# Performance work log

Measured on AMD Instinct MI355X. Metric: run time of the kernel, lower is better.

The kernel has to match this reference:

```python
import jax, jax.numpy as jnp
import numpy as np

DIM = 128      # d_msa
HEADS = 8
DH = 64        # dim_head
INNER = HEADS * DH  # 512
R = 64         # tie_attn_dim (MSA rows)
N = 512        # residues
DPAIR = 128
LN_EPS = 1e-5


def _layernorm(x, g, b):
    mu = jnp.mean(x, axis=-1, keepdims=True)
    var = jnp.mean((x - mu) ** 2, axis=-1, keepdims=True)
    return (x - mu) * jax.lax.rsqrt(var + LN_EPS) * g + b


def setup_inputs() -> dict:
    key = jax.random.key(0)
    ks = jax.random.split(key, 12)
    s = 0.02
    return {
        "x": jax.random.normal(ks[0], (R, N, DIM), jnp.float32),
        "pair_bias": jax.random.normal(ks[1], (1, N, N, DPAIR), jnp.float32),
        "Wq": jax.random.normal(ks[2], (DIM, INNER), jnp.float32) * s,
        "Wkv": jax.random.normal(ks[3], (DIM, 2 * INNER), jnp.float32) * s,
        "Wo": jax.random.normal(ks[4], (INNER, DIM), jnp.float32) * s,
        "bo": jnp.zeros((DIM,), jnp.float32),
        "ln_g": jnp.ones((DPAIR,), jnp.float32),
        "ln_b": jnp.zeros((DPAIR,), jnp.float32),
        "Wpair": jax.random.normal(ks[5], (DPAIR, HEADS), jnp.float32) * s,
        "Wsq": jax.random.normal(ks[6], (DIM, DIM), jnp.float32) * s,
        "bsq": jnp.zeros((DIM,), jnp.float32),
        "Wsk": jax.random.normal(ks[7], (DIM, DIM), jnp.float32) * s,
        "bsk": jnp.zeros((DIM,), jnp.float32),
        "tie_attn_dim": R,
    }


def reference(x, pair_bias, Wq, Wkv, Wo, bo, ln_g, ln_b, Wpair, Wsq, bsq, Wsk, bsk, tie_attn_dim):
    r = tie_attn_dim
    br, n, dim = x.shape
    b = br // r
    h, dh = HEADS, DH
    dsw = dim // h  # per-head dim inside PositionalWiseWeight

    # projections: (b*r, n, inner) -> (b, r, h, n, dh)
    q = (x @ Wq).reshape(b, r, n, h, dh).transpose(0, 1, 3, 2, 4)
    kv = x @ Wkv
    k, v = jnp.split(kv, 2, axis=-1)
    k = k.reshape(b, r, n, h, dh).transpose(0, 1, 3, 2, 4)
    v = v.reshape(b, r, n, h, dh).transpose(0, 1, 3, 2, 4)

    # soft tied row weights (PositionalWiseWeight): w[b, i(pos), h, r]
    m = x.reshape(b, r, n, dim)
    sq = (m[:, :1] @ Wsq + bsq).reshape(b, 1, n, h, dsw).transpose(0, 2, 3, 1, 4)  # b n h 1 d
    sk = (m @ Wsk + bsk).reshape(b, r, n, h, dsw).transpose(0, 2, 3, 1, 4)          # b n h r d
    wlog = jnp.einsum('bnhud,bnhrd->bnhr', sq, sk) / np.float32(np.sqrt(dsw))
    w = jax.nn.softmax(wlog, axis=-1)  # softmax over rows r

    # tied-row attention logits with soft weights
    scale = np.float32(dh) ** -0.5
    dots = jnp.einsum('bihr,brhid,brhjd->bhij', w, q, k) * scale

    # pair bias: LayerNorm + Linear(dim_pair -> heads), broadcast into logits
    pb = _layernorm(pair_bias, ln_g, ln_b) @ Wpair  # (b, i, j, h)
    dots = dots + pb.transpose(0, 3, 1, 2)

    attn = jax.nn.softmax(dots, axis=-1)  # (b, h, i, j)

    out = jnp.einsum('bhij,brhjd->brhid', attn, v)           # (b, r, h, n, dh)
    out = out.transpose(0, 1, 3, 2, 4).reshape(br, n, h * dh)
    out = out @ Wo + bo                                       # (b*r, n, dim)
    return out.reshape(1, br, n, dim)
```

## Files before the change

### kernel.cpp

```cpp
#include <hip/hip_runtime.h>
#include <hip/hip_bf16.h>

typedef unsigned short u16;
typedef unsigned int u32;
typedef __attribute__((ext_vector_type(8))) short short8;
typedef __attribute__((ext_vector_type(4))) float floatx4;

__device__ inline float bf2f(u16 u) { union { u32 i; float f; } v; v.i = ((u32)u) << 16; return v.f; }
__device__ inline u16 f2bf(float f) {
    union { float f; u32 i; } v; v.f = f;
    u32 lsb = (v.i >> 16) & 1u;
    v.i += 0x7fffu + lsb;
    return (u16)(v.i >> 16);
}

__device__ inline uint4 pack8(float4 a, float4 b) {
    uint4 q;
    q.x = (u32)f2bf(a.x) | ((u32)f2bf(a.y) << 16);
    q.y = (u32)f2bf(a.z) | ((u32)f2bf(a.w) << 16);
    q.z = (u32)f2bf(b.x) | ((u32)f2bf(b.y) << 16);
    q.w = (u32)f2bf(b.z) | ((u32)f2bf(b.w) << 16);
    return q;
}

__device__ inline void ld8(u16* dst, const float* src) {
    const float4 a = *(const float4*)src;
    const float4 b = *(const float4*)(src + 4);
    *(uint4*)dst = pack8(a, b);
}

__device__ inline void async16(u16* ldst, const u16* gsrc) {
    __builtin_amdgcn_global_load_lds((const __attribute__((address_space(1))) u32*)gsrc,
                                     (__attribute__((address_space(3))) u32*)ldst, 16, 0, 0);
}

template <int N> __device__ inline void waitvm() {
    static_assert(N == 0 || N == 3 || N == 4 || N == 6 || N == 8, "unsupported vmcnt");
    if constexpr (N == 0) asm volatile("s_waitcnt vmcnt(0)" ::: "memory");
    if constexpr (N == 3) asm volatile("s_waitcnt vmcnt(3)" ::: "memory");
    if constexpr (N == 4) asm volatile("s_waitcnt vmcnt(4)" ::: "memory");
    if constexpr (N == 6) asm volatile("s_waitcnt vmcnt(6)" ::: "memory");
    if constexpr (N == 8) asm volatile("s_waitcnt vmcnt(8)" ::: "memory");
}
__device__ inline void barrier_raw() {
    asm volatile("s_barrier" ::: "memory");
    __builtin_amdgcn_sched_barrier(0);
}
__device__ inline void waitlgkm0() {
    asm volatile("s_waitcnt lgkmcnt(0)" ::: "memory");
    __builtin_amdgcn_sched_barrier(0);
}

template <int BM, int BN, class Epi>
__global__ __launch_bounds__(256) void gemm_nt(const u16* __restrict__ A, const u16* __restrict__ B,
                                               long sAz, long sBz, int lda, int ldb, int K, int zlog, Epi epi)
{
    constexpr int AELE = BM * 32, BELE = BN * 32;
    constexpr int SLOT = AELE + BELE;
    constexpr int IA = BM / 64, IB = BN / 64;
    constexpr int PW = IA + IB;
    constexpr bool STAGE = Epi::chunked;
    static_assert(!STAGE || BN == 128, "chunked epilogue assumes BN=128");
    constexpr int LDC = BN + 4;
    constexpr size_t RB = sizeof(u16) * 4 * (size_t)SLOT;
    constexpr size_t EB = STAGE ? sizeof(float) * 64 * (size_t)LDC : 0;
    constexpr size_t LB = RB > EB ? RB : EB;
    __shared__ __align__(16) char smem[LB];
    u16* lds = (u16*)smem;
    const int tid  = threadIdx.x;
    const int lane = tid & 63;
    const int wave = tid >> 6;
    const int z    = blockIdx.z;
    const int zh   = z >> zlog;
    const int zk   = z & ((1 << zlog) - 1);
    const long row0 = (long)blockIdx.y * BM;
    const long col0 = (long)blockIdx.x * BN;
    const u16* Ab = A + (long)zh * sAz + row0 * lda + (long)zk * K;
    const u16* Bb = B + (long)zh * sBz + col0 * ldb + (long)zk * K;
    constexpr int WM = BM / 2, WN = BN / 2, TM = WM / 16, TN = WN / 16;
    const int wm = (wave >> 1) * WM;
    const int wn = (wave & 1) * WN;
    const int l15 = lane & 15;
    const int quad = lane >> 4;
    const int swz = (l15 >> 1) & 3;

    floatx4 acc[TM][TN];
#pragma unroll
    for (int i = 0; i < TM; i++)
#pragma unroll
        for (int j = 0; j < TN; j++) acc[i][j] = (floatx4){0.f, 0.f, 0.f, 0.f};

    auto stage = [&](int slot, int ki) {
        const int k0 = ki << 5;
        u16* base = lds + slot * SLOT;
#pragma unroll
        for (int i2 = 0; i2 < IA; i2++) {
            int s = wave * (IA * 64) + i2 * 64 + lane;
            int r = s >> 2, c = (s & 3) ^ ((r >> 1) & 3);
            async16(base + (wave * (IA * 64) + i2 * 64) * 8, Ab + (long)r * lda + k0 + c * 8);
        }
        u16* bbase = base + AELE;
#pragma unroll
        for (int i2 = 0; i2 < IB; i2++) {
            int s = wave * (IB * 64) + i2 * 64 + lane;
            int r = s >> 2, c = (s & 3) ^ ((r >> 1) & 3);
            async16(bbase + (wave * (IB * 64) + i2 * 64) * 8, Bb + (long)r * ldb + k0 + c * 8);
        }
    };

    auto compute = [&](int slot) {
        const u16* As = lds + slot * SLOT;
        const u16* Bs = As + AELE;
        short8 af[TM], bfr[TN];
#pragma unroll
        for (int t = 0; t < TM; t++)
            af[t] = *(const short8*)(As + (wm + t * 16 + l15) * 32 + (quad ^ swz) * 8);
#pragma unroll
        for (int t = 0; t < TN; t++)
            bfr[t] = *(const short8*)(Bs + (wn + t * 16 + l15) * 32 + (quad ^ swz) * 8);
        waitlgkm0();
#pragma unroll
        for (int i = 0; i < TM; i++)
#pragma unroll
            for (int j = 0; j < TN; j++)
                acc[i][j] = __builtin_amdgcn_mfma_f32_16x16x32_bf16(af[i], bfr[j], acc[i][j], 0, 0, 0);
    };

    const int nIter = K >> 5;
    stage(0, 0);
    stage(1, 1);
    for (int i = 0; i + 2 < nIter; i++) {
        stage((i + 2) & 3, i + 2);
        waitvm<2 * PW>();
        barrier_raw();
        compute(i & 3);
    }
    waitvm<PW>(); barrier_raw(); compute((nIter - 2) & 3);
    waitvm<0>();  barrier_raw(); compute((nIter - 1) & 3);

    if constexpr (STAGE) {
        float* cs = (float*)smem;
        constexpr int NP = BM / 64;
#pragma unroll
        for (int p = 0; p < NP; p++) {
            __syncthreads();
            if ((wm >> 6) == p) {
                const int lr0 = wm & 63;
#pragma unroll
                for (int i = 0; i < TM; i++)
#pragma unroll
                    for (int j = 0; j < TN; j++)
#pragma unroll
                        for (int r = 0; r < 4; r++)
                            cs[(lr0 + i * 16 + quad * 4 + r) * LDC + wn + j * 16 + l15] = acc[i][j][r];
            }
            __syncthreads();
            constexpr int CPT = (64 * BN) / (256 * 8);
#pragma unroll
            for (int k = 0; k < CPT; k++) {
                int g = k * 256 + tid;
                int row = g >> 4, c8 = (g & 15) * 8;
                const float* pp = cs + row * LDC + c8;
                float4 a = *(const float4*)pp;
                float4 b = *(const float4*)(pp + 4);
                epi.chunk(zh, zk, (int)row0 + p * 64 + row, (int)col0 + c8, a, b);
            }
        }
    } else {
#pragma unroll
        for (int i = 0; i < TM; i++)
#pragma unroll
            for (int j = 0; j < TN; j++)
#pragma unroll
                for (int r = 0; r < 4; r++) {
                    int row = (int)row0 + wm + i * 16 + quad * 4 + r;
                    int col = (int)col0 + wn + j * 16 + l15;
                    epi(zh, zk, row, col, acc[i][j][r]);
                }
    }
}

struct EpiBiasBF {
    static constexpr bool chunked = true;
    u16* C; const float* bias; int ldc;
    __device__ void chunk(int, int, int row, int col, float4 a, float4 b) const {
        const float4* bp = (const float4*)(bias + col);
        float4 b0 = bp[0], b1 = bp[1];
        a.x += b0.x; a.y += b0.y; a.z += b0.z; a.w += b0.w;
        b.x += b1.x; b.y += b1.y; b.z += b1.z; b.w += b1.w;
        *(uint4*)(C + (long)row * ldc + col) = pack8(a, b);
    }
};
struct EpiQ {
    static constexpr bool chunked = true;
    u16* Qw; const float* w;
    __device__ void chunk(int, int, int row, int col, float4 a, float4 b) const {
        int r = row >> 9, i = row & 511, h = col >> 6, d = col & 63;
        float s = w[((long)(i * 8 + h)) * 64 + r] * 0.125f;
        a.x *= s; a.y *= s; a.z *= s; a.w *= s;
        b.x *= s; b.y *= s; b.z *= s; b.w *= s;
        *(uint4*)(Qw + (long)h * 2097152 + (long)i * 4096 + r * 64 + d) = pack8(a, b);
    }
};
struct EpiKV {
    static constexpr bool chunked = true;
    u16* Kp; u16* Vp;
    __device__ void chunk(int, int, int row, int col, float4 a, float4 b) const {
        int r = row >> 9, j = row & 511;
        u16* dst = (col < 512) ? Kp : Vp;
        int c = col & 511;
        int h = c >> 6, d = c & 63;
        *(uint4*)(dst + (long)h * 2097152 + (long)j * 4096 + r * 64 + d) = pack8(a, b);
    }
};
struct EpiDotsAtomic {
    static constexpr bool chunked = false;
    float* pbdots;
    __device__ void operator()(int zh, int, int row, int col, float v) const {
        atomicAdd(pbdots + (long)zh * 262144 + (long)row * 512 + col, v);
    }
};
struct EpiDotsPart {
    static constexpr bool chunked = false;
    float* pbd; float* parts;
    __device__ void operator()(int zh, int zk, int row, int col, float v) const {
        long idx = (long)zh * 262144 + (long)row * 512 + col;
        if (zk == 0) pbd[idx] += v;
        else         parts[(long)(zk - 1) * 2097152 + idx] = v;
    }
};
struct EpiPV {
    static constexpr bool chunked = true;
    u16* O2;
    __device__ void chunk(int zh, int, int row, int col, float4 a, float4 b) const {
        int r = col >> 6, d = col & 63;
        *(uint4*)(O2 + ((long)r * 512 + row) * 512 + zh * 64 + d) = pack8(a, b);
    }
};
struct EpiOut {
    static constexpr bool chunked = true;
    float* out; const float* bo;
    __device__ void chunk(int, int, int row, int col, float4 a, float4 b) const {
        const float4* bp = (const float4*)(bo + col);
        float4 b0 = bp[0], b1 = bp[1];
        a.x += b0.x; a.y += b0.y; a.z += b0.z; a.w += b0.w;
        b.x += b1.x; b.y += b1.y; b.z += b1.z; b.w += b1.w;
        float4* o = (float4*)(out + (long)row * 128 + col);
        o[0] = a; o[1] = b;
    }
};

__global__ __launch_bounds__(256) void f2bf_kernel(const float* __restrict__ src, u16* __restrict__ dst)
{
    long i = ((long)blockIdx.x * 256 + threadIdx.x) * 8;
    ld8(dst + i, src + i);
}

__global__ __launch_bounds__(256) void transpose_to_bf16(const float* __restrict__ src, u16* __restrict__ dst,
                                                         int R, int C)
{
    __shared__ u16 t[32][33];
    int c0 = blockIdx.x * 32, r0 = blockIdx.y * 32;
    int tx = threadIdx.x, ty = threadIdx.y;
#pragma unroll
    for (int i = 0; i < 32; i += 8) t[ty + i][tx] = f2bf(src[(long)(r0 + ty + i) * C + c0 + tx]);
    __syncthreads();
#pragma unroll
    for (int i = 0; i < 32; i += 8) dst[(long)(c0 + ty + i) * R + r0 + tx] = t[tx][ty + i];
}

__global__ __launch_bounds__(256) void transpose64(const u16* __restrict__ src, u16* __restrict__ dst,
                                                   long ss, long ds, int R, int C)
{
    __shared__ __align__(16) u16 t[64][72];
    const u16* s = src + (long)blockIdx.z * ss;
    u16* d = dst + (long)blockIdx.z * ds;
    int c0 = blockIdx.x * 64, r0 = blockIdx.y * 64;
    int tid = threadIdx.x;
    int row = tid >> 3, ch = tid & 7;
#pragma unroll
    for (int p = 0; p < 2; p++) {
        int r = row + p * 32;
        *(uint4*)&t[r][ch * 8] = *(const uint4*)(s + (long)(r0 + r) * C + c0 + ch * 8);
    }
    __syncthreads();
#pragma unroll
    for (int p = 0; p < 2; p++) {
        int cc = row + p * 32;
        u16 tmp[8];
#pragma unroll
        for (int j = 0; j < 8; j++) tmp[j] = t[ch * 8 + j][cc];
        *(uint4*)(d + (long)(c0 + cc) * R + r0 + ch * 8) = *(uint4*)tmp;
    }
}

__global__ __launch_bounds__(256) void rowweight_kernel(const u16* __restrict__ sk, const u16* __restrict__ sq,
                                                        float* __restrict__ w)
{
    int wid = blockIdx.x * 4 + (threadIdx.x >> 6);
    int lane = threadIdx.x & 63;
    int i = wid >> 3, h = wid & 7;
    const u16* sqp = sq + i * 128 + h * 16;
    const u16* skp = sk + ((long)lane * 512 + i) * 128 + h * 16;
    float dot = 0.f;
#pragma unroll
    for (int c = 0; c < 16; c++) dot += bf2f(sqp[c]) * bf2f(skp[c]);
    float logit = dot * 0.25f;
    float m = logit;
#pragma unroll
    for (int o = 32; o > 0; o >>= 1) m = fmaxf(m, __shfl_xor(m, o));
    float e = __expf(logit - m);
    float ssum = e;
#pragma unroll
    for (int o = 32; o > 0; o >>= 1) ssum += __shfl_xor(ssum, o);
    w[(long)wid * 64 + lane] = e / ssum;
}

__global__ __launch_bounds__(256) void pbprep_kernel(const float* __restrict__ g, const float* __restrict__ b,
                                                     const float* __restrict__ Wp, float* __restrict__ Wg,
                                                     float* __restrict__ SB)
{
    int tid = threadIdx.x;
    for (int t = tid; t < 1024; t += 256) Wg[t] = g[t >> 3] * Wp[t];
    if (tid < 16) {
        int h = tid & 7;
        const float* src = (tid < 8) ? g : b;
        float s = 0.f;
        for (int c = 0; c < 128; c++) s += src[c] * Wp[c * 8 + h];
        SB[tid] = s;
    }
}

__global__ __launch_bounds__(256) void pb_kernel(const float* __restrict__ pair, const float* __restrict__ Wg,
                                                 const float* __restrict__ SB, float* __restrict__ pb)
{
    __shared__ __align__(16) float Ls[64 * 132];
    __shared__ float sWg[1024];
    __shared__ float sSB[16];
    int tid = threadIdx.x;
    for (int t = tid; t < 1024; t += 256) sWg[t] = Wg[t];
    if (tid < 16) sSB[tid] = SB[tid];
    long base = (long)blockIdx.x * 8192;
    const float4* src = (const float4*)(pair + base);
#pragma unroll
    for (int k = 0; k < 8; k++) {
        int e = tid + k * 256;
        float4 v = src[e];
        int r = e >> 5, c = (e & 31) << 2;
        *(float4*)(&Ls[r * 132 + c]) = v;
    }
    __syncthreads();
    int r = tid >> 2, sub = tid & 3;
    const float* row = &Ls[r * 132];
    float sum = 0.f, sqs = 0.f;
#pragma unroll
    for (int k = 0; k < 8; k++) {
        float4 v = *(const float4*)(&row[sub * 32 + k * 4]);
        sum += v.x + v.y + v.z + v.w;
        sqs += v.x * v.x + v.y * v.y + v.z * v.z + v.w * v.w;
    }
    sum += __shfl_xor(sum, 1); sqs += __shfl_xor(sqs, 1);
    sum += __shfl_xor(sum, 2); sqs += __shfl_xor(sqs, 2);
    float mu = sum * (1.f / 128.f);
    float var = sqs * (1.f / 128.f) - mu * mu;
    float rstd = rsqrtf(var + 1e-5f);
    int h0 = sub * 2;
    float a0 = 0.f, a1 = 0.f;
#pragma unroll
    for (int k = 0; k < 32; k++) {
        float4 v = *(const float4*)(&row[k * 4]);
        int c = k * 4;
        a0 += v.x * sWg[c * 8 + h0]     + v.y * sWg[(c + 1) * 8 + h0]
            + v.z * sWg[(c + 2) * 8 + h0] + v.w * sWg[(c + 3) * 8 + h0];
        a1 += v.x * sWg[c * 8 + h0 + 1]     + v.y * sWg[(c + 1) * 8 + h0 + 1]
            + v.z * sWg[(c + 2) * 8 + h0 + 1] + v.w * sWg[(c + 3) * 8 + h0 + 1];
    }
    long idx = (long)blockIdx.x * 64 + r;
    pb[(long)h0 * 262144 + idx]       = rstd * (a0 - mu * sSB[h0])     + sSB[8 + h0];
    pb[(long)(h0 + 1) * 262144 + idx] = rstd * (a1 - mu * sSB[h0 + 1]) + sSB[8 + h0 + 1];
}

__global__ __launch_bounds__(256) void softmax_kernel(const float* __restrict__ dots,
                                                      const float* __restrict__ parts, int np,
                                                      u16* __restrict__ attn)
{
    int row = blockIdx.x * 4 + (threadIdx.x >> 6);
    int lane = threadIdx.x & 63;
    long base = (long)row * 512;
    const float* dp = dots + base;
    float v[8];
#pragma unroll
    for (int k = 0; k < 8; k++) v[k] = dp[k * 64 + lane];
    for (int t = 0; t < np; t++) {
        const float* pp = parts + (long)t * 2097152 + base;
#pragma unroll
        for (int k = 0; k < 8; k++) v[k] += pp[k * 64 + lane];
    }
    float m = v[0];
#pragma unroll
    for (int k = 1; k < 8; k++) m = fmaxf(m, v[k]);
#pragma unroll
    for (int o = 32; o > 0; o >>= 1) m = fmaxf(m, __shfl_xor(m, o));
    float s = 0.f;
#pragma unroll
    for (int k = 0; k < 8; k++) { v[k] = __expf(v[k] - m); s += v[k]; }
#pragma unroll
    for (int o = 32; o > 0; o >>= 1) s += __shfl_xor(s, o);
    float inv = 1.f / s;
    u16* ap = attn + (long)row * 512;
#pragma unroll
    for (int k = 0; k < 8; k++) ap[k * 64 + lane] = f2bf(v[k] * inv);
}

extern "C" void kernel_launch(void* const* d_in, const int* in_sizes, int n_in,
                              void* d_out, int out_size, void* d_ws, size_t ws_size,
                              hipStream_t stream)
{
    const float* x    = (const float*)d_in[0];
    const float* pair = (const float*)d_in[1];
    const float* Wq   = (const float*)d_in[2];
    const float* Wkv  = (const float*)d_in[3];
    const float* Wo   = (const float*)d_in[4];
    const float* bo   = (const float*)d_in[5];
    const float* lng  = (const float*)d_in[6];
    const float* lnb  = (const float*)d_in[7];
    const float* Wp   = (const float*)d_in[8];
    const float* Wsq  = (const float*)d_in[9];
    const float* bsq  = (const float*)d_in[10];
    const float* Wsk  = (const float*)d_in[11];
    const float* bsk  = (const float*)d_in[12];
    float* out = (float*)d_out;

    char* ws = (char*)d_ws;
    size_t off = 0;
    auto alloc = [&](size_t bytes) -> char* {
        char* p = ws + off; off += (bytes + 255) & ~(size_t)255; return p;
    };
    u16* WqT  = (u16*)alloc(512 * 128 * 2);
    u16* WkvT = (u16*)alloc(1024 * 128 * 2);
    u16* WskT = (u16*)alloc(128 * 128 * 2);
    u16* WsqT = (u16*)alloc(128 * 128 * 2);
    u16* WoT  = (u16*)alloc(128 * 512 * 2);
    u16* xbf  = (u16*)alloc((size_t)32768 * 128 * 2);
    u16* sk   = (u16*)alloc((size_t)32768 * 128 * 2);
    u16* sq   = (u16*)alloc(512 * 128 * 2);
    float* w  = (float*)alloc((size_t)4096 * 64 * 4);
    float* Wg = (float*)alloc(1024 * 4);
    float* SB = (float*)alloc(16 * 4);
    u16* bufA = (u16*)alloc((size_t)8 * 512 * 4096 * 2);
    u16* bufB = (u16*)alloc((size_t)8 * 512 * 4096 * 2);
    u16* Vt   = (u16*)alloc((size_t)8 * 4096 * 512 * 2);
    float* pbd = (float*)alloc((size_t)8 * 512 * 512 * 4);
    float* parts = (float*)alloc((size_t)3 * 2097152 * 4);
    const bool useParts = (off <= ws_size);
    u16* attn = sk;

    dim3 blk(256);
    dim3 tb(32, 8);

    f2bf_kernel<<<dim3(2048), blk, 0, stream>>>(x, xbf);
    pbprep_kernel<<<dim3(1), blk, 0, stream>>>(lng, lnb, Wp, Wg, SB);

    transpose_to_bf16<<<dim3(16, 4, 1), tb, 0, stream>>>(Wq,  WqT,  128, 512);
    transpose_to_bf16<<<dim3(32, 4, 1), tb, 0, stream>>>(Wkv, WkvT, 128, 1024);
    transpose_to_bf16<<<dim3(4, 4, 1),  tb, 0, stream>>>(Wsk, WskT, 128, 128);
    transpose_to_bf16<<<dim3(4, 4, 1),  tb, 0, stream>>>(Wsq, WsqT, 128, 128);
    transpose_to_bf16<<<dim3(4, 16, 1), tb, 0, stream>>>(Wo,  WoT,  512, 128);

    gemm_nt<64, 128, EpiBiasBF><<<dim3(1, 512, 1), blk, 0, stream>>>(
        xbf, WskT, 0, 0, 128, 128, 128, 0, EpiBiasBF{sk, bsk, 128});
    gemm_nt<64, 128, EpiBiasBF><<<dim3(1, 8, 1), blk, 0, stream>>>(
        xbf, WsqT, 0, 0, 128, 128, 128, 0, EpiBiasBF{sq, bsq, 128});
    rowweight_kernel<<<dim3(1024), blk, 0, stream>>>(sk, sq, w);

    gemm_nt<128, 128, EpiKV><<<dim3(8, 256, 1), blk, 0, stream>>>(
        xbf, WkvT, 0, 0, 128, 128, 128, 0, EpiKV{bufB, bufA});
    transpose64<<<dim3(64, 8, 8), blk, 0, stream>>>(bufA, Vt, 2097152, 2097152, 512, 4096);

    pb_kernel<<<dim3(4096), blk, 0, stream>>>(pair, Wg, SB, pbd);

    gemm_nt<128, 128, EpiQ><<<dim3(4, 256, 1), blk, 0, stream>>>(
        xbf, WqT, 0, 0, 128, 128, 128, 0, EpiQ{bufA, w});

    if (useParts) {
        gemm_nt<128, 128, EpiDotsPart><<<dim3(4, 4, 32), blk, 0, stream>>>(
            bufA, bufB, 2097152, 2097152, 4096, 4096, 1024, 2, EpiDotsPart{pbd, parts});
        softmax_kernel<<<dim3(1024), blk, 0, stream>>>(pbd, parts, 3, attn);
    } else {
        gemm_nt<128, 128, EpiDotsAtomic><<<dim3(4, 4, 64), blk, 0, stream>>>(
            bufA, bufB, 2097152, 2097152, 4096, 4096, 512, 3, EpiDotsAtomic{pbd});
        softmax_kernel<<<dim3(1024), blk, 0, stream>>>(pbd, pbd, 0, attn);
    }

    gemm_nt<128, 128, EpiPV><<<dim3(32, 4, 8), blk, 0, stream>>>(
        attn, Vt, 262144, 2097152, 512, 512, 512, 0, EpiPV{bufB});

    gemm_nt<64, 128, EpiOut><<<dim3(1, 512, 1), blk, 0, stream>>>(
        bufB, WoT, 0, 0, 512, 512, 512, 0, EpiOut{out, bo});
}
```

Baseline: 418.2 us.

## Fuse prep kernels, merge Sk/Sq GEMMs, write V transposed from KV epilogue

Folds the bf16 conversion, the five weight transposes and the pair-bias prep into one prep kernel. Runs the Sk and Sq projections as a single launch, with the Sq blocks beyond row 8 exiting early. The KV GEMM epilogue now writes V directly in transposed layout through a column-major LDS stage, which removes the separate transpose64 pass and its round trip of V through memory. This cuts launch count and memory traffic, at the cost of more complex epilogue branching and a strided LDS staging pattern.

```diff
diff --git a/kernel.cpp b/kernel.cpp
--- a/kernel.cpp
+++ b/kernel.cpp
@@ -63,7 +63,9 @@
     static_assert(!STAGE || BN == 128, "chunked epilogue assumes BN=128");
     constexpr int LDC = BN + 4;
     constexpr size_t RB = sizeof(u16) * 4 * (size_t)SLOT;
-    constexpr size_t EB = STAGE ? sizeof(float) * 64 * (size_t)LDC : 0;
+    constexpr size_t EBR = STAGE ? sizeof(float) * 64 * (size_t)LDC : 0;
+    constexpr size_t EBV = (STAGE && Epi::kv) ? sizeof(float) * 128 * 68 : 0;
+    constexpr size_t EB = EBR > EBV ? EBR : EBV;
     constexpr size_t LB = RB > EB ? RB : EB;
     __shared__ __align__(16) char smem[LB];
     u16* lds = (u16*)smem;
@@ -73,6 +75,9 @@
     const int z    = blockIdx.z;
     const int zh   = z >> zlog;
     const int zk   = z & ((1 << zlog) - 1);
+    if constexpr (Epi::ylim >= 0) {
+        if (zh != 0 && (int)blockIdx.y >= Epi::ylim) return;
+    }
     const long row0 = (long)blockIdx.y * BM;
     const long col0 = (long)blockIdx.x * BN;
     const u16* Ab = A + (long)zh * sAz + row0 * lda + (long)zk * K;
@@ -141,29 +146,56 @@
     if constexpr (STAGE) {
         float* cs = (float*)smem;
         constexpr int NP = BM / 64;
+        bool vtile = false;
+        if constexpr (Epi::kv) vtile = (col0 >= 512);
 #pragma unroll
         for (int p = 0; p < NP; p++) {
             __syncthreads();
-            if ((wm >> 6) == p) {
-                const int lr0 = wm & 63;
-#pragma unroll
-                for (int i = 0; i < TM; i++)
-#pragma unroll
-                    for (int j = 0; j < TN; j++)
-#pragma unroll
-                        for (int r = 0; r < 4; r++)
-                            cs[(lr0 + i * 16 + quad * 4 + r) * LDC + wn + j * 16 + l15] = acc[i][j][r];
+            if (!vtile) {
+                if ((wm >> 6) == p) {
+                    const int lr0 = wm & 63;
+#pragma unroll
+                    for (int i = 0; i < TM; i++)
+#pragma unroll
+                        for (int j = 0; j < TN; j++)
+#pragma unroll
+                            for (int r = 0; r < 4; r++)
+                                cs[(lr0 + i * 16 + quad * 4 + r) * LDC + wn + j * 16 + l15] = acc[i][j][r];
+                }
+                __syncthreads();
+                constexpr int CPT = (64 * BN) / (256 * 8);
+#pragma unroll
+                for (int k = 0; k < CPT; k++) {
+                    int g = k * 256 + tid;
+                    int row = g >> 4, c8 = (g & 15) * 8;
+                    const float* pp = cs + row * LDC + c8;
+                    float4 a = *(const float4*)pp;
+                    float4 b = *(const float4*)(pp + 4);
+                    epi.chunk(zh, zk, (int)row0 + p * 64 + row, (int)col0 + c8, a, b);
+                }
             }
-            __syncthreads();
-            constexpr int CPT = (64 * BN) / (256 * 8);
-#pragma unroll
-            for (int k = 0; k < CPT; k++) {
-                int g = k * 256 + tid;
-                int row = g >> 4, c8 = (g & 15) * 8;
-                const float* pp = cs + row * LDC + c8;
-                float4 a = *(const float4*)pp;
-                float4 b = *(const float4*)(pp + 4);
-                epi.chunk(zh, zk, (int)row0 + p * 64 + row, (int)col0 + c8, a, b);
+            if constexpr (Epi::kv) {
+                if (vtile) {
+                    if ((wm >> 6) == p) {
+                        const int lr0 = wm & 63;
+#pragma unroll
+                        for (int i = 0; i < TM; i++)
+#pragma unroll
+                            for (int j = 0; j < TN; j++)
+                                *(float4*)&cs[(wn + j * 16 + l15) * 68 + lr0 + i * 16 + quad * 4] =
+                                    (float4){acc[i][j][0], acc[i][j][1], acc[i][j][2], acc[i][j][3]};
+                    }
+                    __syncthreads();
+#pragma unroll
+                    for (int k = 0; k < 4; k++) {
+                        int q = k * 256 + tid;
+                        int colL = q >> 3, rg = q & 7;
+                        const float* pp = cs + colL * 68 + rg * 8;
+                        float4 a = *(const float4*)pp;
+                        float4 b = *(const float4*)(pp + 4);
+                        epi.vchunk(zh, (int)row0 + p * 64 + rg * 8, (int)col0 + colL, a, b);
+                    }
+                }
             }
         }
     } else {
@@ -180,19 +212,25 @@
     }
 }
 
-struct EpiBiasBF {
+struct EpiSkSq {
     static constexpr bool chunked = true;
-    u16* C; const float* bias; int ldc;
-    __device__ void chunk(int, int, int row, int col, float4 a, float4 b) const {
+    static constexpr bool kv = false;
+    static constexpr int ylim = 8;
+    u16* sk; u16* sq; const float* bsk; const float* bsq;
+    __device__ void chunk(int zh, int, int row, int col, float4 a, float4 b) const {
+        const float* bias = zh ? bsq : bsk;
+        u16* C = zh ? sq : sk;
         const float4* bp = (const float4*)(bias + col);
         float4 b0 = bp[0], b1 = bp[1];
         a.x += b0.x; a.y += b0.y; a.z += b0.z; a.w += b0.w;
         b.x += b1.x; b.y += b1.y; b.z += b1.z; b.w += b1.w;
-        *(uint4*)(C + (long)row * ldc + col) = pack8(a, b);
+        *(uint4*)(C + (long)row * 128 + col) = pack8(a, b);
     }
 };
 struct EpiQ {
     static constexpr bool chunked = true;
+    static constexpr bool kv = false;
+    static constexpr int ylim = -1;
     u16* Qw; const float* w;
     __device__ void chunk(int, int, int row, int col, float4 a, float4 b) const {
         int r = row >> 9, i = row & 511, h = col >> 6, d = col & 63;
@@ -204,17 +242,24 @@
 };
 struct EpiKV {
     static constexpr bool chunked = true;
-    u16* Kp; u16* Vp;
+    static constexpr bool kv = true;
+    static constexpr int ylim = -1;
+    u16* Kp; u16* Vt;
     __device__ void chunk(int, int, int row, int col, float4 a, float4 b) const {
         int r = row >> 9, j = row & 511;
-        u16* dst = (col < 512) ? Kp : Vp;
-        int c = col & 511;
-        int h = c >> 6, d = c & 63;
-        *(uint4*)(dst + (long)h * 2097152 + (long)j * 4096 + r * 64 + d) = pack8(a, b);
+        int h = col >> 6, d = col & 63;
+        *(uint4*)(Kp + (long)h * 2097152 + (long)j * 4096 + r * 64 + d) = pack8(a, b);
+    }
+    __device__ void vchunk(int, int row8, int col, float4 a, float4 b) const {
+        int r = row8 >> 9, j0 = row8 & 511;
+        int c = col - 512, h = c >> 6, d = c & 63;
+        *(uint4*)(Vt + (long)h * 2097152 + ((long)r * 64 + d) * 512 + j0) = pack8(a, b);
     }
 };
 struct EpiDotsAtomic {
     static constexpr bool chunked = false;
+    static constexpr bool kv = false;
+    static constexpr int ylim = -1;
     float* pbdots;
     __device__ void operator()(int zh, int, int row, int col, float v) const {
         atomicAdd(pbdots + (long)zh * 262144 + (long)row * 512 + col, v);
@@ -222,6 +267,8 @@
 };
 struct EpiDotsPart {
     static constexpr bool chunked = false;
+    static constexpr bool kv = false;
+    static constexpr int ylim = -1;
     float* pbd; float* parts;
     __device__ void operator()(int zh, int zk, int row, int col, float v) const {
         long idx = (long)zh * 262144 + (long)row * 512 + col;
@@ -231,6 +278,8 @@
 };
 struct EpiPV {
     static constexpr bool chunked = true;
+    static constexpr bool kv = false;
+    static constexpr int ylim = -1;
     u16* O2;
     __device__ void chunk(int zh, int, int row, int col, float4 a, float4 b) const {
         int r = col >> 6, d = col & 63;
@@ -239,6 +288,8 @@
 };
 struct EpiOut {
     static constexpr bool chunked = true;
+    static constexpr bool kv = false;
+    static constexpr int ylim = -1;
     float* out; const float* bo;
     __device__ void chunk(int, int, int row, int col, float4 a, float4 b) const {
         const float4* bp = (const float4*)(bo + col);
@@ -250,18 +301,12 @@
     }
 };
 
-__global__ __launch_bounds__(256) void f2bf_kernel(const float* __restrict__ src, u16* __restrict__ dst)
-{
-    long i = ((long)blockIdx.x * 256 + threadIdx.x) * 8;
-    ld8(dst + i, src + i);
-}
-
-__global__ __launch_bounds__(256) void transpose_to_bf16(const float* __restrict__ src, u16* __restrict__ dst,
-                                                         int R, int C)
+__device__ inline void trans_dev(const float* __restrict__ src, u16* __restrict__ dst,
+                                 int R, int C, int bx, int by, int tid)
 {
     __shared__ u16 t[32][33];
-    int c0 = blockIdx.x * 32, r0 = blockIdx.y * 32;
-    int tx = threadIdx.x, ty = threadIdx.y;
+    int c0 = bx * 32, r0 = by * 32;
+    int tx = tid & 31, ty = tid >> 5;
 #pragma unroll
     for (int i = 0; i < 32; i += 8) t[ty + i][tx] = f2bf(src[(long)(r0 + ty + i) * C + c0 + tx]);
     __syncthreads();
@@ -269,58 +314,28 @@
     for (int i = 0; i < 32; i += 8) dst[(long)(c0 + ty + i) * R + r0 + tx] = t[tx][ty + i];
 }
 
-__global__ __launch_bounds__(256) void transpose64(const u16* __restrict__ src, u16* __restrict__ dst,
-                                                   long ss, long ds, int R, int C)
-{
-    __shared__ __align__(16) u16 t[64][72];
-    const u16* s = src + (long)blockIdx.z * ss;
-    u16* d = dst + (long)blockIdx.z * ds;
-    int c0 = blockIdx.x * 64, r0 = blockIdx.y * 64;
-    int tid = threadIdx.x;
-    int row = tid >> 3, ch = tid & 7;
-#pragma unroll
-    for (int p = 0; p < 2; p++) {
-        int r = row + p * 32;
-        *(uint4*)&t[r][ch * 8] = *(const uint4*)(s + (long)(r0 + r) * C + c0 + ch * 8);
-    }
-    __syncthreads();
-#pragma unroll
-    for (int p = 0; p < 2; p++) {
-        int cc = row + p * 32;
-        u16 tmp[8];
-#pragma unroll
-        for (int j = 0; j < 8; j++) tmp[j] = t[ch * 8 + j][cc];
-        *(uint4*)(d + (long)(c0 + cc) * R + r0 + ch * 8) = *(uint4*)tmp;
-    }
-}
-
-__global__ __launch_bounds__(256) void rowweight_kernel(const u16* __restrict__ sk, const u16* __restrict__ sq,
-                                                        float* __restrict__ w)
-{
-    int wid = blockIdx.x * 4 + (threadIdx.x >> 6);
-    int lane = threadIdx.x & 63;
-    int i = wid >> 3, h = wid & 7;
-    const u16* sqp = sq + i * 128 + h * 16;
-    const u16* skp = sk + ((long)lane * 512 + i) * 128 + h * 16;
-    float dot = 0.f;
-#pragma unroll
-    for (int c = 0; c < 16; c++) dot += bf2f(sqp[c]) * bf2f(skp[c]);
-    float logit = dot * 0.25f;
-    float m = logit;
-#pragma unroll
-    for (int o = 32; o > 0; o >>= 1) m = fmaxf(m, __shfl_xor(m, o));
-    float e = __expf(logit - m);
-    float ssum = e;
-#pragma unroll
-    for (int o = 32; o > 0; o >>= 1) ssum += __shfl_xor(ssum, o);
-    w[(long)wid * 64 + lane] = e / ssum;
-}
-
-__global__ __launch_bounds__(256) void pbprep_kernel(const float* __restrict__ g, const float* __restrict__ b,
-                                                     const float* __restrict__ Wp, float* __restrict__ Wg,
-                                                     float* __restrict__ SB)
-{
-    int tid = threadIdx.x;
+__global__ __launch_bounds__(256) void prep_kernel(
+    const float* __restrict__ x, u16* __restrict__ xbf,
+    const float* __restrict__ Wq, u16* __restrict__ WqT,
+    const float* __restrict__ Wkv, u16* __restrict__ WkvT,
+    const float* __restrict__ Wsk, u16* __restrict__ WskT,
+    const float* __restrict__ Wsq, u16* __restrict__ WsqT,
+    const float* __restrict__ Wo, u16* __restrict__ WoT,
+    const float* __restrict__ g, const float* __restrict__ b,
+    const float* __restrict__ Wp, float* __restrict__ Wg, float* __restrict__ SB)
+{
+    int gb = blockIdx.x, tid = threadIdx.x;
+    if (gb < 2048) { long i = ((long)gb * 256 + tid) * 8; ld8(xbf + i, x + i); return; }
+    gb -= 2048;
+    if (gb < 64)  { trans_dev(Wq,  WqT,  128, 512,  gb & 15, gb >> 4, tid); return; }
+    gb -= 64;
+    if (gb < 128) { trans_dev(Wkv, WkvT, 128, 1024, gb & 31, gb >> 5, tid); return; }
+    gb -= 128;
+    if (gb < 16)  { trans_dev(Wsk, WskT, 128, 128,  gb & 3,  gb >> 2, tid); return; }
+    gb -= 16;
+    if (gb < 16)  { trans_dev(Wsq, WsqT, 128, 128,  gb & 3,  gb >> 2, tid); return; }
+    gb -= 16;
+    if (gb < 64)  { trans_dev(Wo,  WoT,  512, 128,  gb & 3,  gb >> 2, tid); return; }
     for (int t = tid; t < 1024; t += 256) Wg[t] = g[t >> 3] * Wp[t];
     if (tid < 16) {
         int h = tid & 7;
@@ -329,6 +344,28 @@
         for (int c = 0; c < 128; c++) s += src[c] * Wp[c * 8 + h];
         SB[tid] = s;
     }
+}
+
+__global__ __launch_bounds__(256) void rowweight_kernel(const u16* __restrict__ sk, const u16* __restrict__ sq,
+                                                        float* __restrict__ w)
+{
+    int wid = blockIdx.x * 4 + (threadIdx.x >> 6);
+    int lane = threadIdx.x & 63;
+    int i = wid >> 3, h = wid & 7;
+    const u16* sqp = sq + i * 128 + h * 16;
+    const u16* skp = sk + ((long)lane * 512 + i) * 128 + h * 16;
+    float dot = 0.f;
+#pragma unroll
+    for (int c = 0; c < 16; c++) dot += bf2f(sqp[c]) * bf2f(skp[c]);
+    float logit = dot * 0.25f;
+    float m = logit;
+#pragma unroll
+    for (int o = 32; o > 0; o >>= 1) m = fmaxf(m, __shfl_xor(m, o));
+    float e = __expf(logit - m);
+    float ssum = e;
+#pragma unroll
+    for (int o = 32; o > 0; o >>= 1) ssum += __shfl_xor(ssum, o);
+    w[(long)wid * 64 + lane] = e / ssum;
 }
 
 __global__ __launch_bounds__(256) void pb_kernel(const float* __restrict__ pair, const float* __restrict__ Wg,
@@ -456,26 +493,17 @@
     u16* attn = sk;
 
     dim3 blk(256);
-    dim3 tb(32, 8);
-
-    f2bf_kernel<<<dim3(2048), blk, 0, stream>>>(x, xbf);
-    pbprep_kernel<<<dim3(1), blk, 0, stream>>>(lng, lnb, Wp, Wg, SB);
-
-    transpose_to_bf16<<<dim3(16, 4, 1), tb, 0, stream>>>(Wq,  WqT,  128, 512);
-    transpose_to_bf16<<<dim3(32, 4, 1), tb, 0, stream>>>(Wkv, WkvT, 128, 1024);
-    transpose_to_bf16<<<dim3(4, 4, 1),  tb, 0, stream>>>(Wsk, WskT, 128, 128);
-    transpose_to_bf16<<<dim3(4, 4, 1),  tb, 0, stream>>>(Wsq, WsqT, 128, 128);
-    transpose_to_bf16<<<dim3(4, 16, 1), tb, 0, stream>>>(Wo,  WoT,  512, 128);
-
-    gemm_nt<64, 128, EpiBiasBF><<<dim3(1, 512, 1), blk, 0, stream>>>(
-        xbf, WskT, 0, 0, 128, 128, 128, 0, EpiBiasBF{sk, bsk, 128});
-    gemm_nt<64, 128, EpiBiasBF><<<dim3(1, 8, 1), blk, 0, stream>>>(
-        xbf, WsqT, 0, 0, 128, 128, 128, 0, EpiBiasBF{sq, bsq, 128});
+
+    prep_kernel<<<dim3(2337), blk, 0, stream>>>(x, xbf, Wq, WqT, Wkv, WkvT,
+                                                Wsk, WskT, Wsq, WsqT, Wo, WoT,
+                                                lng, lnb, Wp, Wg, SB);
+
+    gemm_nt<64, 128, EpiSkSq><<<dim3(1, 512, 2), blk, 0, stream>>>(
+        xbf, WskT, 0, 16384, 128, 128, 128, 0, EpiSkSq{sk, sq, bsk, bsq});
     rowweight_kernel<<<dim3(1024), blk, 0, stream>>>(sk, sq, w);
 
     gemm_nt<128, 128, EpiKV><<<dim3(8, 256, 1), blk, 0, stream>>>(
-        xbf, WkvT, 0, 0, 128, 128, 128, 0, EpiKV{bufB, bufA});
-    transpose64<<<dim3(64, 8, 8), blk, 0, stream>>>(bufA, Vt, 2097152, 2097152, 512, 4096);
+        xbf, WkvT, 0, 0, 128, 128, 128, 0, EpiKV{bufB, Vt});
 
     pb_kernel<<<dim3(4096), blk, 0, stream>>>(pair, Wg, SB, pbd);
 
```

New measurement: 392.9 us. -6.0%, faster.
